# Kernel tuning notes

Hardware: AMD Instinct MI355X
Metric: run time of the kernel (lower is better)

Reference implementation:

```python
import jax, jax.numpy as jnp
import numpy as np

ALPHA = 0.01  # leaky_relu slope (forward default)

def _hist_entropy(x, bins):
    """Mean over batch of per-sample histogram entropy, matching
    np.histogram(sample, bins=bins) + entropy_calc(hist, bw=bins):
      H = -sum(p*log(p)) - log(1/bins) = -sum(p*log(p)) + log(bins).
    x: [B, D] float."""
    B, D = x.shape
    xmin = jnp.min(x, axis=1, keepdims=True)
    xmax = jnp.max(x, axis=1, keepdims=True)
    width = xmax - xmin
    safe_w = jnp.where(width > 0, width, 1.0)
    # np.histogram: equal-width bins over [min, max]; max value goes in last bin
    idx = jnp.floor((x - xmin) / safe_w * bins).astype(jnp.int32)
    idx = jnp.clip(idx, 0, bins - 1)
    flat = (jnp.arange(B, dtype=jnp.int32)[:, None] * bins + idx).reshape(-1)
    counts = jnp.zeros(B * bins, jnp.float32).at[flat].add(1.0).reshape(B, bins)
    p = counts / jnp.float32(D)
    plogp = jnp.where(p > 0, p * jnp.log(jnp.where(p > 0, p, 1.0)), 0.0)
    H = -jnp.sum(plogp, axis=1) + jnp.log(jnp.float32(bins))  # [B]
    return jnp.mean(H)

def _lin(x, W, b):
    return x @ W.T + b

def setup_inputs() -> dict:
    key = jax.random.key(0)
    ks = jax.random.split(key, 13)
    B = 65536
    dims = [(784, 256), (256, 128), (128, 128), (128, 128), (128, 32), (32, 10)]
    inp = {"x": jax.random.normal(ks[0], (B, 784), dtype=jnp.float32)}
    for i, (din, dout) in enumerate(dims):
        s = 1.0 / np.sqrt(din)
        inp[f"W{i+1}"] = jax.random.uniform(ks[1 + 2 * i], (dout, din), jnp.float32, -s, s)
        inp[f"b{i+1}"] = jax.random.uniform(ks[2 + 2 * i], (dout,), jnp.float32, -s, s)
    return inp

def reference(x, W1, b1, W2, b2, W3, b3, W4, b4, W5, b5, W6, b6):
    x = x.reshape(-1, 784)
    Hs = []
    for (W, b) in [(W1, b1), (W2, b2), (W3, b3), (W4, b4), (W5, b5)]:
        x = jax.nn.leaky_relu(_lin(x, W, b), ALPHA)
        Hs.append(_hist_entropy(x, x.shape[1]))  # bins = dim / bin_ratio(=1)
    x = jax.nn.relu(_lin(x, W6, b6))
    out = jax.nn.log_softmax(x, axis=1)
    return (out, Hs[0], Hs[1], Hs[2], Hs[3], Hs[4])
```

## Files before the change

### kernel.cpp

```cpp
#include <hip/hip_runtime.h>
#include <hip/hip_bf16.h>
#include <math.h>

#define ALPHA 0.01f

typedef __bf16 bf16x8 __attribute__((ext_vector_type(8)));
typedef float  floatx4 __attribute__((ext_vector_type(4)));

static __device__ __forceinline__ unsigned short f2bf_bits(float f) {
    return __builtin_bit_cast(unsigned short, (__bf16)f);
}
static __device__ __forceinline__ float bf2f(unsigned short u) {
    return __builtin_bit_cast(float, (unsigned)u << 16);
}

static __device__ __forceinline__ void glds16(const void* g, void* l) {
    __builtin_amdgcn_global_load_lds(
        (const __attribute__((address_space(1))) unsigned int*)g,
        (__attribute__((address_space(3))) unsigned int*)l, 16, 0, 0);
}

template <int CTRL>
static __device__ __forceinline__ float dppmov(float x) {
    int r = __builtin_amdgcn_update_dpp(0, __builtin_bit_cast(int, x), CTRL, 0xf, 0xf, false);
    return __builtin_bit_cast(float, r);
}
static __device__ __forceinline__ float red16min(float x) {
    x = fminf(x, dppmov<0x121>(x)); x = fminf(x, dppmov<0x122>(x));
    x = fminf(x, dppmov<0x124>(x)); x = fminf(x, dppmov<0x128>(x));
    return x;
}
static __device__ __forceinline__ float red16max(float x) {
    x = fmaxf(x, dppmov<0x121>(x)); x = fmaxf(x, dppmov<0x122>(x));
    x = fmaxf(x, dppmov<0x124>(x)); x = fmaxf(x, dppmov<0x128>(x));
    return x;
}
static __device__ __forceinline__ float red16sum(float x) {
    x += dppmov<0x121>(x); x += dppmov<0x122>(x);
    x += dppmov<0x124>(x); x += dppmov<0x128>(x);
    return x;
}

template <int DOUT>
static __device__ __forceinline__ float entropy_tile(const floatx4* acc,
        unsigned int* cc, int lane16)
{
    constexpr int CTN   = DOUT / 16;
    constexpr int HALF  = DOUT / 2;
    constexpr int LOG2D = (DOUT == 256) ? 8 : (DOUT == 128) ? 7 : 5;
    constexpr float LOGB = (DOUT == 256) ? 5.54517744f
                         : (DOUT == 128) ? 4.85203026f : 3.46573590f;
    float Hq = 0.0f;
    #pragma unroll
    for (int reg = 0; reg < 4; reg++) {
        float mn = acc[0][reg], mx = mn;
        #pragma unroll
        for (int ct = 1; ct < CTN; ct++) {
            mn = fminf(mn, acc[ct][reg]);
            mx = fmaxf(mx, acc[ct][reg]);
        }
        mn = red16min(mn);
        mx = red16max(mx);
        float wdt = mx - mn;
        float scale = (float)DOUT / (wdt > 0.0f ? wdt : 1.0f);

        #pragma unroll
        for (int i = 0; i < DOUT / 32; i++) cc[lane16 + 16 * i] = 0u;

        #pragma unroll
        for (int ct = 0; ct < CTN; ct++) {
            int b = (int)((acc[ct][reg] - mn) * scale);
            b = b < (DOUT - 1) ? b : (DOUT - 1);
            atomicAdd(&cc[b & (HALF - 1)],
                      1u << (((b >> (LOG2D - 1)) & 1) << 4));
        }

        float s = 0.0f;
        #pragma unroll
        for (int i = 0; i < DOUT / 32; i++) {
            unsigned int word = cc[lane16 + 16 * i];
            int c0 = (int)(word & 0xffffu), c1 = (int)(word >> 16);
            if (c0 > 0) { float p = (float)c0 * (1.0f / (float)DOUT); s += p * __logf(p); }
            if (c1 > 0) { float p = (float)c1 * (1.0f / (float)DOUT); s += p * __logf(p); }
        }
        s = red16sum(s);
        Hq += LOGB - s;
    }
    Hq += __shfl_xor(Hq, 16, 64);
    Hq += __shfl_xor(Hq, 32, 64);
    return Hq;
}

template <int DIN, int DOUT>
static __device__ __forceinline__ float tail_layer(const bf16x8* a,
    char* __restrict__ yt,
    const unsigned short* __restrict__ Wf, const float* __restrict__ bias,
    unsigned int* __restrict__ cc, int lane)
{
    constexpr int KT = DIN / 32, CTN = DOUT / 16, NCO = DOUT / 8;
    const int lane16 = lane & 15, q = lane >> 4;

    floatx4 acc[CTN];
    #pragma unroll
    for (int ct = 0; ct < CTN; ct++) acc[ct] = (floatx4)(0.0f);

    #pragma unroll
    for (int kt = 0; kt < KT; kt++) {
        #pragma unroll
        for (int ct = 0; ct < CTN; ct++) {
            bf16x8 bw = *(const bf16x8*)(Wf + ((size_t)(kt * CTN + ct) * 64 + lane) * 8);
            acc[ct] = __builtin_amdgcn_mfma_f32_16x16x32_bf16(a[kt], bw, acc[ct], 0, 0, 0);
        }
    }

    #pragma unroll
    for (int ct = 0; ct < CTN; ct++) {
        float bb = bias[ct * 16 + lane16];
        #pragma unroll
        for (int reg = 0; reg < 4; reg++) {
            float v = acc[ct][reg] + bb;
            v = v > 0.0f ? v : ALPHA * v;
            acc[ct][reg] = v;
            int r  = q * 4 + reg;
            int c  = (ct * 16 + lane16) >> 3;
            int cs = c ^ (r & (NCO - 1));
            *(unsigned short*)(yt + r * (DOUT * 2) + cs * 16 + (lane16 & 7) * 2)
                = f2bf_bits(v);
        }
    }
    return entropy_tile<DOUT>(acc, cc, lane16);
}

template <int DIN>
static __device__ __forceinline__ void load_afrags(bf16x8* a,
    const char* __restrict__ yt, int lane16, int q)
{
    constexpr int KT = DIN / 32, NCI = DIN / 8;
    asm volatile("s_waitcnt lgkmcnt(0)" ::: "memory");
    #pragma unroll
    for (int kt = 0; kt < KT; kt++) {
        int cs = (kt * 4 + q) ^ (lane16 & (NCI - 1));
        a[kt] = *(const bf16x8*)(yt + lane16 * (DIN * 2) + cs * 16);
    }
    asm volatile("s_waitcnt lgkmcnt(0)" ::: "memory");
}

__global__ __launch_bounds__(256, 4) void mega(
    const float* __restrict__ X,
    const unsigned short* __restrict__ W1f, const float* __restrict__ b1,
    const unsigned short* __restrict__ W2f, const float* __restrict__ b2,
    const unsigned short* __restrict__ W3f, const float* __restrict__ b3,
    const unsigned short* __restrict__ W4f, const float* __restrict__ b4,
    const unsigned short* __restrict__ W5f, const float* __restrict__ b5,
    const float* __restrict__ W6, const float* __restrict__ b6,
    float* __restrict__ out, float* __restrict__ Hpart)
{
    __shared__ __align__(16) char regA[24576];
    __shared__ unsigned int cnt[16][129];
    __shared__ float hsum[4];

    const int t = threadIdx.x;
    const int lane = t & 63, lane16 = lane & 15, q = lane >> 4, w = t >> 6;
    const int row0 = blockIdx.x * 64;
    const int myrow = w * 16 + lane16;
    unsigned int* cc = cnt[w * 4 + q];
    char* yt = regA + w * 4096;

    floatx4 acc1[16];
    #pragma unroll
    for (int ct = 0; ct < 16; ct++) acc1[ct] = (floatx4)(0.0f);
    {
        constexpr int DIN = 784, CTN = 16, KT_FULL = 24;
        char* smemX = regA;
        char* smemW = regA + 8192;

        auto stageW = [&](int kt) {
            #pragma unroll
            for (int j = w; j < CTN; j += 4)
                glds16(W1f + ((size_t)kt * CTN * 64 + j * 64 + lane) * 8,
                       smemW + j * 64 * 16);
        };
        auto stageX = [&](int kt) {
            #pragma unroll
            for (int j = 0; j < 2; j++) {
                int s  = w * 128 + j * 64 + lane;
                int gc = (s & ~7) | ((s ^ (s >> 3)) & 7);
                int r  = gc >> 3, c = gc & 7;
                glds16(X + (size_t)(row0 + r) * DIN + kt * 32 + c * 4,
                       smemX + (w * 128 + j * 64) * 16);
            }
        };
        auto compute = [&]() {
            int s0 = myrow * 8 + (((2 * q)     ^ myrow) & 7);
            int s1 = myrow * 8 + (((2 * q + 1) ^ myrow) & 7);
            float4 f0 = *(const float4*)(smemX + s0 * 16);
            float4 f1 = *(const float4*)(smemX + s1 * 16);
            uint4 pk;
            pk.x = (unsigned)f2bf_bits(f0.x) | ((unsigned)f2bf_bits(f0.y) << 16);
            pk.y = (unsigned)f2bf_bits(f0.z) | ((unsigned)f2bf_bits(f0.w) << 16);
            pk.z = (unsigned)f2bf_bits(f1.x) | ((unsigned)f2bf_bits(f1.y) << 16);
            pk.w = (unsigned)f2bf_bits(f1.z) | ((unsigned)f2bf_bits(f1.w) << 16);
            bf16x8 a = __builtin_bit_cast(bf16x8, pk);
            #pragma unroll
            for (int ct = 0; ct < CTN; ct++) {
                bf16x8 bw = *(const bf16x8*)(smemW + (ct * 64 + lane) * 16);
                acc1[ct] = __builtin_amdgcn_mfma_f32_16x16x32_bf16(a, bw, acc1[ct], 0, 0, 0);
            }
        };

        #pragma unroll 1
        for (int kt = 0; kt < KT_FULL; kt++) {
            __syncthreads();
            stageX(kt);
            stageW(kt);
            __syncthreads();
            compute();
        }
        __syncthreads();
        stageW(KT_FULL);
        {
            int r = t >> 2, c = t & 3;
            float4 v = *(const float4*)(X + (size_t)(row0 + r) * DIN
                                        + KT_FULL * 32 + c * 4);
            *(float4*)(smemX + (r * 8 + ((c ^ r) & 7)) * 16) = v;
            int c2 = c + 4;
            *(float4*)(smemX + (r * 8 + ((c2 ^ r) & 7)) * 16)
                = make_float4(0.f, 0.f, 0.f, 0.f);
        }
        __syncthreads();
        compute();
    }

    #pragma unroll
    for (int ct = 0; ct < 16; ct++) {
        float bb = b1[ct * 16 + lane16];
        #pragma unroll
        for (int reg = 0; reg < 4; reg++) {
            float v = acc1[ct][reg] + bb;
            acc1[ct][reg] = v > 0.0f ? v : ALPHA * v;
        }
    }

    float H1 = entropy_tile<256>(acc1, cc, lane16);
    if (lane == 0) hsum[w] = H1;
    __syncthreads();
    if (t == 0) Hpart[blockIdx.x] = hsum[0] + hsum[1] + hsum[2] + hsum[3];

    bf16x8 a2[8];
    #pragma unroll
    for (int p = 0; p < 2; p++) {
        #pragma unroll
        for (int ct = 0; ct < 8; ct++) {
            #pragma unroll
            for (int reg = 0; reg < 4; reg++) {
                int r  = q * 4 + reg;
                int c  = (ct * 16 + lane16) >> 3;
                int cs = c ^ r;
                *(unsigned short*)(yt + r * 256 + cs * 16 + (lane16 & 7) * 2)
                    = f2bf_bits(acc1[p * 8 + ct][reg]);
            }
        }
        asm volatile("s_waitcnt lgkmcnt(0)" ::: "memory");
        #pragma unroll
        for (int kt = 0; kt < 4; kt++) {
            int cs = (kt * 4 + q) ^ lane16;
            a2[p * 4 + kt] = *(const bf16x8*)(yt + lane16 * 256 + cs * 16);
        }
        asm volatile("s_waitcnt lgkmcnt(0)" ::: "memory");
    }

    float H = tail_layer<256, 128>(a2, yt, W2f, b2, cc, lane);
    if (lane == 0) Hpart[1 * 4096 + blockIdx.x * 4 + w] = H;

    bf16x8 a[4];
    load_afrags<128>(a, yt, lane16, q);
    H = tail_layer<128, 128>(a, yt, W3f, b3, cc, lane);
    if (lane == 0) Hpart[2 * 4096 + blockIdx.x * 4 + w] = H;

    load_afrags<128>(a, yt, lane16, q);
    H = tail_layer<128, 128>(a, yt, W4f, b4, cc, lane);
    if (lane == 0) Hpart[3 * 4096 + blockIdx.x * 4 + w] = H;

    load_afrags<128>(a, yt, lane16, q);
    H = tail_layer<128, 32>(a, yt, W5f, b5, cc, lane);
    if (lane == 0) Hpart[4 * 4096 + blockIdx.x * 4 + w] = H;

    asm volatile("s_waitcnt lgkmcnt(0)" ::: "memory");
    float x6[32];
    #pragma unroll
    for (int c = 0; c < 4; c++) {
        int cs = c ^ (lane16 & 3);
        bf16x8 v = *(const bf16x8*)(yt + lane16 * 64 + cs * 16);
        #pragma unroll
        for (int j = 0; j < 8; j++) x6[c * 8 + j] = (float)v[j];
    }

    float z[3];
    float m = -1e30f;
    #pragma unroll
    for (int s2 = 0; s2 < 3; s2++) {
        int jj = q * 3 + s2;
        float a6 = 0.0f;
        if (jj < 10) {
            a6 = b6[jj];
            #pragma unroll
            for (int k = 0; k < 32; k++) a6 = fmaf(x6[k], W6[jj * 32 + k], a6);
            a6 = fmaxf(a6, 0.0f);
            m = fmaxf(m, a6);
        }
        z[s2] = a6;
    }
    m = fmaxf(m, __shfl_xor(m, 16, 64));
    m = fmaxf(m, __shfl_xor(m, 32, 64));
    float se = 0.0f;
    #pragma unroll
    for (int s2 = 0; s2 < 3; s2++)
        if (q * 3 + s2 < 10) se += __expf(z[s2] - m);
    se += __shfl_xor(se, 16, 64);
    se += __shfl_xor(se, 32, 64);
    float ls = __logf(se);
    const size_t ro = (size_t)(row0 + w * 16 + lane16) * 10;
    #pragma unroll
    for (int s2 = 0; s2 < 3; s2++) {
        int jj = q * 3 + s2;
        if (jj < 10) out[ro + jj] = z[s2] - m - ls;
    }
}

__global__ void convert_wfrag(const float* __restrict__ W1, const float* __restrict__ W2,
                              const float* __restrict__ W3, const float* __restrict__ W4,
                              const float* __restrict__ W5, unsigned short* __restrict__ out)
{
    int s = blockIdx.x * 256 + threadIdx.x;
    if (s >= 34304) return;
    const float* W; int DIN, CTN, sl;
    if      (s < 25600) { W = W1; DIN = 784; CTN = 16; sl = s;         }
    else if (s < 29696) { W = W2; DIN = 256; CTN = 8;  sl = s - 25600; }
    else if (s < 31744) { W = W3; DIN = 128; CTN = 8;  sl = s - 29696; }
    else if (s < 33792) { W = W4; DIN = 128; CTN = 8;  sl = s - 31744; }
    else                { W = W5; DIN = 128; CTN = 2;  sl = s - 33792; }
    int kt = sl / (CTN * 64);
    int ct = (sl / 64) % CTN;
    int ln = sl & 63;
    int r  = ct * 16 + (ln & 15);
    int k0 = kt * 32 + (ln >> 4) * 8;
    unsigned short v[8];
    #pragma unroll
    for (int j = 0; j < 8; j++) {
        int k = k0 + j;
        v[j] = (k < DIN) ? f2bf_bits(W[(size_t)r * DIN + k]) : (unsigned short)0;
    }
    uint4 pk;
    pk.x = (unsigned)v[0] | ((unsigned)v[1] << 16);
    pk.y = (unsigned)v[2] | ((unsigned)v[3] << 16);
    pk.z = (unsigned)v[4] | ((unsigned)v[5] << 16);
    pk.w = (unsigned)v[6] | ((unsigned)v[7] << 16);
    *(uint4*)(out + (size_t)s * 8) = pk;
}

__global__ __launch_bounds__(256) void hreduce(const float* __restrict__ Hp,
                                               float* __restrict__ out_tail)
{
    __shared__ float sm[4];
    const int t = threadIdx.x, lane = t & 63, w = t >> 6;
    const int l = blockIdx.x;
    const int n = l ? 4096 : 1024;
    const float* p = Hp + (size_t)l * 4096;
    float s = 0.0f;
    for (int i = t; i < n; i += 256) s += p[i];
    #pragma unroll
    for (int off = 1; off <= 32; off <<= 1) s += __shfl_xor(s, off, 64);
    if (lane == 0) sm[w] = s;
    __syncthreads();
    if (t == 0)
        out_tail[l] = (sm[0] + sm[1] + sm[2] + sm[3]) * (1.0f / 65536.0f);
}

extern "C" void kernel_launch(void* const* d_in, const int* in_sizes, int n_in,
                              void* d_out, int out_size, void* d_ws, size_t ws_size,
                              hipStream_t stream)
{
    const float* x  = (const float*)d_in[0];
    const float* W1 = (const float*)d_in[1];  const float* b1 = (const float*)d_in[2];
    const float* W2 = (const float*)d_in[3];  const float* b2 = (const float*)d_in[4];
    const float* W3 = (const float*)d_in[5];  const float* b3 = (const float*)d_in[6];
    const float* W4 = (const float*)d_in[7];  const float* b4 = (const float*)d_in[8];
    const float* W5 = (const float*)d_in[9];  const float* b5 = (const float*)d_in[10];
    const float* W6 = (const float*)d_in[11]; const float* b6 = (const float*)d_in[12];
    float* out = (float*)d_out;

    constexpr int B = 65536;
    char* ws = (char*)d_ws;
    float* Hpart = (float*)ws;
    unsigned short* Wfrag = (unsigned short*)(ws + 81920);
    unsigned short* W1f = Wfrag;
    unsigned short* W2f = W1f + 25600 * 8;
    unsigned short* W3f = W2f + 4096 * 8;
    unsigned short* W4f = W3f + 2048 * 8;
    unsigned short* W5f = W4f + 2048 * 8;

    convert_wfrag<<<134, 256, 0, stream>>>(W1, W2, W3, W4, W5, Wfrag);

    mega<<<B / 64, 256, 0, stream>>>(
        x, W1f, b1, W2f, b2, W3f, b3, W4f, b4, W5f, b5, W6, b6, out, Hpart);

    hreduce<<<5, 256, 0, stream>>>(Hpart, out + (size_t)B * 10);
}
```

Baseline: 401.6 us.

## Load layer-1 operands directly from global, dropping LDS staging and block barriers

Layer 1 now reads X rows and pre-swizzled W1 fragments straight from global memory into registers, with a one-step register prefetch of X. This replaces the LDS staging via global_load_lds and the two __syncthreads per K-step. Biases are folded into the accumulator initialisation, and the layer-1 entropy partial is written per wave, which removes a block barrier. The trade-off is that every wave reloads W1 from global or L2 instead of sharing one LDS copy, and X loads per lane are less coalesced.

New measurement: 408.2 us. Within noise of the previous version (+1.7%).

```diff
diff --git a/kernel.cpp b/kernel.cpp
--- a/kernel.cpp
+++ b/kernel.cpp
@@ -9,15 +9,6 @@
 
 static __device__ __forceinline__ unsigned short f2bf_bits(float f) {
     return __builtin_bit_cast(unsigned short, (__bf16)f);
-}
-static __device__ __forceinline__ float bf2f(unsigned short u) {
-    return __builtin_bit_cast(float, (unsigned)u << 16);
-}
-
-static __device__ __forceinline__ void glds16(const void* g, void* l) {
-    __builtin_amdgcn_global_load_lds(
-        (const __attribute__((address_space(1))) unsigned int*)g,
-        (__attribute__((address_space(3))) unsigned int*)l, 16, 0, 0);
 }
 
 template <int CTRL>
@@ -39,6 +30,15 @@
     x += dppmov<0x121>(x); x += dppmov<0x122>(x);
     x += dppmov<0x124>(x); x += dppmov<0x128>(x);
     return x;
+}
+
+static __device__ __forceinline__ uint4 pack8(float4 f0, float4 f1) {
+    uint4 pk;
+    pk.x = (unsigned)f2bf_bits(f0.x) | ((unsigned)f2bf_bits(f0.y) << 16);
+    pk.y = (unsigned)f2bf_bits(f0.z) | ((unsigned)f2bf_bits(f0.w) << 16);
+    pk.z = (unsigned)f2bf_bits(f1.x) | ((unsigned)f2bf_bits(f1.y) << 16);
+    pk.w = (unsigned)f2bf_bits(f1.z) | ((unsigned)f2bf_bits(f1.w) << 16);
+    return pk;
 }
 
 template <int DOUT>
@@ -102,7 +102,7 @@
 
     floatx4 acc[CTN];
     #pragma unroll
-    for (int ct = 0; ct < CTN; ct++) acc[ct] = (floatx4)(0.0f);
+    for (int ct = 0; ct < CTN; ct++) acc[ct] = (floatx4)(bias[ct * 16 + lane16]);
 
     #pragma unroll
     for (int kt = 0; kt < KT; kt++) {
@@ -115,10 +115,9 @@
 
     #pragma unroll
     for (int ct = 0; ct < CTN; ct++) {
-        float bb = bias[ct * 16 + lane16];
         #pragma unroll
         for (int reg = 0; reg < 4; reg++) {
-            float v = acc[ct][reg] + bb;
+            float v = acc[ct][reg];
             v = v > 0.0f ? v : ALPHA * v;
             acc[ct][reg] = v;
             int r  = q * 4 + reg;
@@ -155,96 +154,58 @@
     const float* __restrict__ W6, const float* __restrict__ b6,
     float* __restrict__ out, float* __restrict__ Hpart)
 {
-    __shared__ __align__(16) char regA[24576];
+    __shared__ __align__(16) char yts[4][4096];
     __shared__ unsigned int cnt[16][129];
-    __shared__ float hsum[4];
 
     const int t = threadIdx.x;
     const int lane = t & 63, lane16 = lane & 15, q = lane >> 4, w = t >> 6;
     const int row0 = blockIdx.x * 64;
     const int myrow = w * 16 + lane16;
     unsigned int* cc = cnt[w * 4 + q];
-    char* yt = regA + w * 4096;
+    char* yt = yts[w];
+    const int hidx = blockIdx.x * 4 + w;
 
     floatx4 acc1[16];
     #pragma unroll
-    for (int ct = 0; ct < 16; ct++) acc1[ct] = (floatx4)(0.0f);
+    for (int ct = 0; ct < 16; ct++) acc1[ct] = (floatx4)(b1[ct * 16 + lane16]);
     {
-        constexpr int DIN = 784, CTN = 16, KT_FULL = 24;
-        char* smemX = regA;
-        char* smemW = regA + 8192;
-
-        auto stageW = [&](int kt) {
+        const float* Xr = X + (size_t)(row0 + myrow) * 784;
+        float4 fa0 = *(const float4*)(Xr + q * 8);
+        float4 fa1 = *(const float4*)(Xr + q * 8 + 4);
+        #pragma unroll 1
+        for (int kt = 0; kt < 24; kt++) {
+            bf16x8 a = __builtin_bit_cast(bf16x8, pack8(fa0, fa1));
+            int noff = (kt == 23) ? ((q & 1) * 8) : (q * 8);
+            const float* nsrc = Xr + (kt + 1) * 32 + noff;
+            fa0 = *(const float4*)(nsrc);
+            fa1 = *(const float4*)(nsrc + 4);
             #pragma unroll
-            for (int j = w; j < CTN; j += 4)
-                glds16(W1f + ((size_t)kt * CTN * 64 + j * 64 + lane) * 8,
-                       smemW + j * 64 * 16);
-        };
-        auto stageX = [&](int kt) {
-            #pragma unroll
-            for (int j = 0; j < 2; j++) {
-                int s  = w * 128 + j * 64 + lane;
-                int gc = (s & ~7) | ((s ^ (s >> 3)) & 7);
-                int r  = gc >> 3, c = gc & 7;
-                glds16(X + (size_t)(row0 + r) * DIN + kt * 32 + c * 4,
-                       smemX + (w * 128 + j * 64) * 16);
-            }
-        };
-        auto compute = [&]() {
-            int s0 = myrow * 8 + (((2 * q)     ^ myrow) & 7);
-            int s1 = myrow * 8 + (((2 * q + 1) ^ myrow) & 7);
-            float4 f0 = *(const float4*)(smemX + s0 * 16);
-            float4 f1 = *(const float4*)(smemX + s1 * 16);
-            uint4 pk;
-            pk.x = (unsigned)f2bf_bits(f0.x) | ((unsigned)f2bf_bits(f0.y) << 16);
-            pk.y = (unsigned)f2bf_bits(f0.z) | ((unsigned)f2bf_bits(f0.w) << 16);
-            pk.z = (unsigned)f2bf_bits(f1.x) | ((unsigned)f2bf_bits(f1.y) << 16);
-            pk.w = (unsigned)f2bf_bits(f1.z) | ((unsigned)f2bf_bits(f1.w) << 16);
-            bf16x8 a = __builtin_bit_cast(bf16x8, pk);
-            #pragma unroll
-            for (int ct = 0; ct < CTN; ct++) {
-                bf16x8 bw = *(const bf16x8*)(smemW + (ct * 64 + lane) * 16);
+            for (int ct = 0; ct < 16; ct++) {
+                bf16x8 bw = *(const bf16x8*)(W1f + ((size_t)(kt * 16 + ct) * 64 + lane) * 8);
                 acc1[ct] = __builtin_amdgcn_mfma_f32_16x16x32_bf16(a, bw, acc1[ct], 0, 0, 0);
             }
-        };
-
-        #pragma unroll 1
-        for (int kt = 0; kt < KT_FULL; kt++) {
-            __syncthreads();
-            stageX(kt);
-            stageW(kt);
-            __syncthreads();
-            compute();
-        }
-        __syncthreads();
-        stageW(KT_FULL);
-        {
-            int r = t >> 2, c = t & 3;
-            float4 v = *(const float4*)(X + (size_t)(row0 + r) * DIN
-                                        + KT_FULL * 32 + c * 4);
-            *(float4*)(smemX + (r * 8 + ((c ^ r) & 7)) * 16) = v;
-            int c2 = c + 4;
-            *(float4*)(smemX + (r * 8 + ((c2 ^ r) & 7)) * 16)
-                = make_float4(0.f, 0.f, 0.f, 0.f);
-        }
-        __syncthreads();
-        compute();
+        }
+        uint4 pk = pack8(fa0, fa1);
+        if (q >= 2) { pk.x = 0u; pk.y = 0u; pk.z = 0u; pk.w = 0u; }
+        bf16x8 a = __builtin_bit_cast(bf16x8, pk);
+        #pragma unroll
+        for (int ct = 0; ct < 16; ct++) {
+            bf16x8 bw = *(const bf16x8*)(W1f + ((size_t)(24 * 16 + ct) * 64 + lane) * 8);
+            acc1[ct] = __builtin_amdgcn_mfma_f32_16x16x32_bf16(a, bw, acc1[ct], 0, 0, 0);
+        }
     }
 
     #pragma unroll
     for (int ct = 0; ct < 16; ct++) {
-        float bb = b1[ct * 16 + lane16];
         #pragma unroll
         for (int reg = 0; reg < 4; reg++) {
-            float v = acc1[ct][reg] + bb;
+            float v = acc1[ct][reg];
             acc1[ct][reg] = v > 0.0f ? v : ALPHA * v;
         }
     }
 
-    float H1 = entropy_tile<256>(acc1, cc, lane16);
-    if (lane == 0) hsum[w] = H1;
-    __syncthreads();
-    if (t == 0) Hpart[blockIdx.x] = hsum[0] + hsum[1] + hsum[2] + hsum[3];
+    float H = entropy_tile<256>(acc1, cc, lane16);
+    if (lane == 0) Hpart[0 * 4096 + hidx] = H;
 
     bf16x8 a2[8];
     #pragma unroll
@@ -269,21 +230,21 @@
         asm volatile("s_waitcnt lgkmcnt(0)" ::: "memory");
     }
 
-    float H = tail_layer<256, 128>(a2, yt, W2f, b2, cc, lane);
-    if (lane == 0) Hpart[1 * 4096 + blockIdx.x * 4 + w] = H;
+    H = tail_layer<256, 128>(a2, yt, W2f, b2, cc, lane);
+    if (lane == 0) Hpart[1 * 4096 + hidx] = H;
 
     bf16x8 a[4];
     load_afrags<128>(a, yt, lane16, q);
     H = tail_layer<128, 128>(a, yt, W3f, b3, cc, lane);
-    if (lane == 0) Hpart[2 * 4096 + blockIdx.x * 4 + w] = H;
+    if (lane == 0) Hpart[2 * 4096 + hidx] = H;
 
     load_afrags<128>(a, yt, lane16, q);
     H = tail_layer<128, 128>(a, yt, W4f, b4, cc, lane);
-    if (lane == 0) Hpart[3 * 4096 + blockIdx.x * 4 + w] = H;
+    if (lane == 0) Hpart[3 * 4096 + hidx] = H;
 
     load_afrags<128>(a, yt, lane16, q);
     H = tail_layer<128, 32>(a, yt, W5f, b5, cc, lane);
-    if (lane == 0) Hpart[4 * 4096 + blockIdx.x * 4 + w] = H;
+    if (lane == 0) Hpart[4 * 4096 + hidx] = H;
 
     asm volatile("s_waitcnt lgkmcnt(0)" ::: "memory");
     float x6[32];
@@ -364,10 +325,9 @@
     __shared__ float sm[4];
     const int t = threadIdx.x, lane = t & 63, w = t >> 6;
     const int l = blockIdx.x;
-    const int n = l ? 4096 : 1024;
     const float* p = Hp + (size_t)l * 4096;
     float s = 0.0f;
-    for (int i = t; i < n; i += 256) s += p[i];
+    for (int i = t; i < 4096; i += 256) s += p[i];
     #pragma unroll
     for (int off = 1; off <= 32; off <<= 1) s += __shfl_xor(s, off, 64);
     if (lane == 0) sm[w] = s;
```
